# Kernel tuning notes

Hardware: AMD Instinct MI355X
Metric: run time of the kernel (lower is better)

Reference implementation:

```python
import jax, jax.numpy as jnp
import numpy as np
import math

D = 768      # inp_dim
NH = 8       # head_num
DH = 96      # head_dim
HID = NH * DH  # 768
P = 2 * D    # up_l proj dim = 1536
K = 4        # conv kernel size
CAP = 15.0   # gate soft cap
EPS = 1e-6


def layer_norm(x, w, b, eps=EPS):
    mu = jnp.mean(x, axis=-1, keepdims=True)
    var = jnp.mean((x - mu) ** 2, axis=-1, keepdims=True)
    return (x - mu) / jnp.sqrt(var + eps) * w + b


def softcap(v, cap=CAP):
    return cap * jnp.tanh(v / cap)


def setup_inputs() -> dict:
    key = jax.random.key(0)
    ks = jax.random.split(key, 8)
    B, S = 8, 2048
    x = jax.random.normal(ks[0], (B, S, D), dtype=jnp.float32)
    # scaled inits (1/sqrt(fan_in)) for numerical sanity
    up_l_w = jax.random.normal(ks[1], (P, D), dtype=jnp.float32) / math.sqrt(D)
    up_r_w = jax.random.normal(ks[2], (HID, D), dtype=jnp.float32) / math.sqrt(D)
    conv_w = jax.random.normal(ks[3], (K,), dtype=jnp.float32) / math.sqrt(K)
    skip_w = jax.random.normal(ks[4], (HID, P), dtype=jnp.float32) / math.sqrt(P)
    fused_w = jax.random.normal(ks[5], (2 * NH + 4 * HID, P), dtype=jnp.float32) / math.sqrt(P)
    fused_b = jnp.zeros((2 * NH + 4 * HID,), dtype=jnp.float32)
    down_w = jax.random.normal(ks[6], (D, HID), dtype=jnp.float32) / math.sqrt(HID)
    return {
        'x': x,
        'ln_w': jnp.ones((D,), jnp.float32), 'ln_b': jnp.zeros((D,), jnp.float32),
        'up_l_w': up_l_w, 'up_r_w': up_r_w, 'conv_w': conv_w, 'skip_w': skip_w,
        'fused_w': fused_w, 'fused_b': fused_b,
        'hid_w': jnp.ones((HID,), jnp.float32), 'hid_b': jnp.zeros((HID,), jnp.float32),
        'down_w': down_w,
    }


def reference(x, ln_w, ln_b, up_l_w, up_r_w, conv_w, skip_w, fused_w, fused_b, hid_w, hid_b, down_w):
    B, S, _ = x.shape
    dt = x.dtype
    inv_sqrt_dh = 1.0 / math.sqrt(DH)

    # ---- per-timestep-independent precomputation (vectorized over B,S) ----
    x_n = layer_norm(x, ln_w, ln_b)                       # [B,S,D]
    xl = jnp.einsum('bsd,pd->bsp', x_n, up_l_w)           # [B,S,P]
    r = jnp.einsum('bsd,hd->bsh', x_n, up_r_w)            # [B,S,HID]
    # causal conv over the FEATURE dim (Conv1d(1,1,K) applied to x_t.unsqueeze(1))
    xpad = jnp.pad(xl, ((0, 0), (0, 0), (K - 1, 0)))
    xc = conv_w[0] * xpad[..., 0:P]
    for t in range(1, K):
        xc = xc + conv_w[t] * xpad[..., t:t + P]
    xc = jax.nn.silu(xc)                                  # [B,S,P]
    x_skip = jnp.einsum('bsp,hp->bsh', xc, skip_w)        # [B,S,HID]
    z = jnp.einsum('bsp,op->bso', xc, fused_w) + fused_b  # [B,S,3088]
    i_g = softcap(z[..., :NH])                            # [B,S,NH]
    f_g = softcap(z[..., NH:2 * NH])                      # [B,S,NH]
    o = jax.nn.sigmoid(z[..., 2 * NH:2 * NH + HID])       # [B,S,HID]
    q = z[..., 2 * NH + HID:2 * NH + 2 * HID].reshape(B, S, NH, DH)
    k = z[..., 2 * NH + 2 * HID:2 * NH + 3 * HID].reshape(B, S, NH, DH) * inv_sqrt_dh
    v = z[..., 2 * NH + 3 * HID:].reshape(B, S, NH, DH)

    # ---- sequential matrix-state recurrence over time ----
    def step(carry, inp):
        c, n, m = carry
        it, ft, ot, qt, kt, vt, skipt, rt, xt = inp
        m_t = jnp.maximum(ft + m, it)                     # [B,NH]
        ig = jnp.exp(it - m_t)
        fg = jnp.exp(ft - m_t + m)
        c = fg[..., None, None] * c + ig[..., None, None] * jnp.einsum('bhd,bhe->bhde', vt, kt)
        n = fg[..., None] * n + ig[..., None] * kt
        num = jnp.einsum('bhde,bhe->bhd', c, qt)          # [B,NH,DH]
        den = jnp.maximum(jnp.sum(n * qt, axis=-1, keepdims=True), 1.0)
        h = ot * (num / den).reshape(B, HID)
        out = layer_norm(h, hid_w, hid_b) + skipt
        out = out * jax.nn.silu(rt)
        out = jnp.einsum('bh,dh->bd', out, down_w) + xt
        return (c, n, m_t), out

    tm = lambda a: jnp.swapaxes(a, 0, 1)  # time-major
    carry0 = (jnp.zeros((B, NH, DH, DH), dt), jnp.ones((B, NH, DH), dt), jnp.zeros((B, NH), dt))
    xs = (tm(i_g), tm(f_g), tm(o), tm(q), tm(k), tm(v), tm(x_skip), tm(r), tm(x))
    _, outs = jax.lax.scan(step, carry0, xs)
    return jnp.swapaxes(outs, 0, 1)  # [B,S,D]
```

## Files before the change

kernel.cpp:

```cpp
#include <hip/hip_runtime.h>
#include <hip/hip_bf16.h>

#define D_    768
#define P_    1536
#define HID_  768
#define NH_   8
#define DH_   96
#define S_    2048
#define LCH   256
#define NCH   8

typedef __hip_bfloat16 bf16_t;
typedef __attribute__((ext_vector_type(8))) short s16x8;
typedef __attribute__((ext_vector_type(8))) unsigned short u16x8;
typedef __attribute__((ext_vector_type(4))) float f32x4;

__device__ __forceinline__ float b2f(unsigned short u) {
    union { unsigned int i; float f; } x; x.i = ((unsigned int)u) << 16; return x.f;
}
__device__ __forceinline__ unsigned short f2b(float f) {
    bf16_t h = __float2bfloat16(f);
    unsigned short u; __builtin_memcpy(&u, &h, 2); return u;
}
__device__ __forceinline__ bf16_t u2b(unsigned short u) {
    bf16_t t; __builtin_memcpy(&t, &u, 2); return t;
}

__device__ __forceinline__ void gload16(const void* g, const void* l) {
    __builtin_amdgcn_global_load_lds(
        (const __attribute__((address_space(1))) unsigned int*)(unsigned long long)(g),
        (__attribute__((address_space(3))) unsigned int*)(unsigned int)(unsigned long long)(l),
        16, 0, 0);
}

__global__ void cvt_kernel(const float* __restrict__ src, bf16_t* __restrict__ dst, int n) {
    int i = blockIdx.x * blockDim.x + threadIdx.x;
    int stride = gridDim.x * blockDim.x;
    for (; i < n; i += stride) dst[i] = __float2bfloat16(src[i]);
}

__global__ void cvt2_kernel(const float* __restrict__ src, bf16_t* __restrict__ hi,
                            bf16_t* __restrict__ lo, int n) {
    int i = blockIdx.x * blockDim.x + threadIdx.x;
    int stride = gridDim.x * blockDim.x;
    for (; i < n; i += stride) {
        float x = src[i];
        bf16_t h = __float2bfloat16(x);
        hi[i] = h;
        lo[i] = __float2bfloat16(x - __bfloat162float(h));
    }
}

__global__ __launch_bounds__(256) void ln_x_kernel(const float* __restrict__ x,
                                                   const float* __restrict__ w,
                                                   const float* __restrict__ b,
                                                   bf16_t* __restrict__ xn) {
    const int t = blockIdx.x, tid = threadIdx.x;
    const size_t rb = (size_t)t * D_;
    float v0 = x[rb + tid], v1 = x[rb + tid + 256], v2 = x[rb + tid + 512];
    float sm = v0 + v1 + v2;
    float sq = v0 * v0 + v1 * v1 + v2 * v2;
#pragma unroll
    for (int off = 32; off > 0; off >>= 1) { sm += __shfl_xor(sm, off); sq += __shfl_xor(sq, off); }
    __shared__ float ws4[8];
    const int wid = tid >> 6, lane = tid & 63;
    if (lane == 0) { ws4[wid] = sm; ws4[4 + wid] = sq; }
    __syncthreads();
    sm = ws4[0] + ws4[1] + ws4[2] + ws4[3];
    sq = ws4[4] + ws4[5] + ws4[6] + ws4[7];
    const float mu = sm * (1.f / D_);
    const float rs = rsqrtf(sq * (1.f / D_) - mu * mu + 1e-6f);
    bf16_t* row = xn + (size_t)t * 1536;
#pragma unroll
    for (int k2 = 0; k2 < 3; ++k2) {
        const int c = tid + k2 * 256;
        const float v = (k2 == 0 ? v0 : k2 == 1 ? v1 : v2);
        const float y = (v - mu) * rs * w[c] + b[c];
        bf16_t h = __float2bfloat16(y);
        row[c] = h;
        row[768 + c] = __float2bfloat16(y - __bfloat162float(h));
    }
}

__global__ __launch_bounds__(192) void conv_gate_kernel(const float* __restrict__ xl,
                                                        const float* __restrict__ cw,
                                                        const float* __restrict__ fw,
                                                        const float* __restrict__ fb,
                                                        bf16_t* __restrict__ xch,
                                                        float* __restrict__ gates) {
    const int t = blockIdx.x, c = threadIdx.x;
    const float* row = xl + (size_t)t * P_;
    const float4* r4 = (const float4*)row;
    float4 a = r4[2 * c], b4 = r4[2 * c + 1];
    float pm3 = 0.f, pm2 = 0.f, pm1 = 0.f;
    if (c > 0) { pm3 = row[c * 8 - 3]; pm2 = row[c * 8 - 2]; pm1 = row[c * 8 - 1]; }
    const float w0 = cw[0], w1 = cw[1], w2 = cw[2], w3 = cw[3];
    float xv[11] = {pm3, pm2, pm1, a.x, a.y, a.z, a.w, b4.x, b4.y, b4.z, b4.w};
    float xc[8];
    u16x8 h8;
#pragma unroll
    for (int j = 0; j < 8; ++j) {
        float s = w0 * xv[j] + w1 * xv[j + 1] + w2 * xv[j + 2] + w3 * xv[j + 3];
        s = s * (1.f / (1.f + __expf(-s)));
        xc[j] = s;
        h8[j] = f2b(s);
    }
    *(u16x8*)(xch + (size_t)t * P_ + c * 8) = h8;

    float pj[16];
#pragma unroll
    for (int j = 0; j < 16; ++j) {
        const float* wr = fw + (size_t)j * P_ + c * 8;
        float p = 0.f;
#pragma unroll
        for (int u = 0; u < 8; ++u) p += xc[u] * wr[u];
        pj[j] = p;
    }
#pragma unroll
    for (int j = 0; j < 16; ++j)
#pragma unroll
        for (int off = 32; off > 0; off >>= 1) pj[j] += __shfl_xor(pj[j], off);
    __shared__ float red[3][16];
    const int wv = c >> 6, ln = c & 63;
    if (ln == 0) {
#pragma unroll
        for (int j = 0; j < 16; ++j) red[wv][j] = pj[j];
    }
    __syncthreads();
    if (c < 16) {
        const float z = red[0][c] + red[1][c] + red[2][c] + fb[c];
        gates[(size_t)t * 16 + c] = 15.f * tanhf(z * (1.f / 15.f));
    }
}

template <int NPASS, int MODE, int KTP>
__global__ __launch_bounds__(512, 2) void gemm256(
    const char* __restrict__ Ab, int astride, int aloff,
    const bf16_t* __restrict__ Wh, const bf16_t* __restrict__ Wl,
    bf16_t* __restrict__ out0, float* __restrict__ outf, int ldout,
    bf16_t* __restrict__ p1, bf16_t* __restrict__ p2,
    bf16_t* __restrict__ p3, bf16_t* __restrict__ p4,
    const float* __restrict__ bias, const float* __restrict__ resid) {
    __shared__ char smem[131072];
    const int tid = threadIdx.x;
    const int gx = gridDim.x;
    int flat = blockIdx.y * gx + blockIdx.x;
    const int cpx = (gx * gridDim.y) >> 3;
    flat = (flat & 7) * cpx + (flat >> 3);
    const int nt = flat % gx, mt = flat / gx;
    const int wid = tid >> 6, lane = tid & 63;
    const int wm = wid >> 2, wn = wid & 3;
    const int l15 = lane & 15, l4 = lane >> 4;
    const int sw = l15 & 7;
    constexpr int VT = NPASS * KTP;
    const size_t wstride = (size_t)KTP * 128;

    auto stage = [&](int h) {
        const int t = h >> 2;
        if (t >= VT) return;
        const int m = h & 3;
        const int pass = t / KTP;
        const int k0b = (t - pass * KTP) << 7;
        char* ldsdst = smem + (size_t)(h & 7) * 16384;
        const char* src;
        size_t stride;
        if (m < 2) {
            src = Ab + (pass == 2 ? aloff : 0) + (size_t)(mt * 256 + m * 128) * astride + k0b;
            stride = (size_t)astride;
        } else {
            const bf16_t* wp = (pass == 1) ? Wl : Wh;
            src = (const char*)wp + (size_t)(nt * 256 + (m - 2) * 128) * wstride + k0b;
            stride = wstride;
        }
        const int r0 = tid >> 3, cd = tid & 7;
#pragma unroll
        for (int l = 0; l < 2; ++l) {
            const int row = l * 64 + r0;
            gload16(src + (size_t)row * stride + (size_t)((cd ^ (row & 7)) << 4),
                    ldsdst + l * 8192 + tid * 16);
        }
    };

    f32x4 acc[8][4];
#pragma unroll
    for (int i = 0; i < 8; ++i)
#pragma unroll
        for (int j = 0; j < 4; ++j) acc[i][j] = f32x4{0.f, 0.f, 0.f, 0.f};

#pragma unroll
    for (int h = 0; h < 6; ++h) stage(h);
    asm volatile("s_waitcnt vmcnt(4)" ::: "memory");
    __builtin_amdgcn_s_barrier();

    s16x8 a03[4][2], a47[4][2], bb[2][2];

    for (int vt = 0; vt < VT; ++vt) {
        const char* ldsA = smem + (vt & 1) * 65536 + wm * 16384;
        const char* ldsB = smem + (vt & 1) * 65536 + 32768 + (wn >> 1) * 16384;
        const int brb = (wn & 1) * 64;
        const int hb = vt * 4 + 6;

#pragma unroll
        for (int i = 0; i < 4; ++i) {
            const int row = i * 16 + l15;
#pragma unroll
            for (int kk = 0; kk < 2; ++kk)
                a03[i][kk] = *(const s16x8*)(ldsA + row * 128 + ((((kk << 2) | l4) ^ sw) << 4));
        }
#pragma unroll
        for (int j = 0; j < 2; ++j) {
            const int row = brb + j * 16 + l15;
#pragma unroll
            for (int kk = 0; kk < 2; ++kk)
                bb[j][kk] = *(const s16x8*)(ldsB + row * 128 + ((((kk << 2) | l4) ^ sw) << 4));
        }
        stage(hb + 0);
        __builtin_amdgcn_s_barrier();
        __builtin_amdgcn_s_setprio(1);
#pragma unroll
        for (int i = 0; i < 4; ++i)
#pragma unroll
            for (int j = 0; j < 2; ++j)
#pragma unroll
                for (int kk = 0; kk < 2; ++kk)
                    acc[i][j] = __builtin_amdgcn_mfma_f32_16x16x32_bf16(a03[i][kk], bb[j][kk], acc[i][j], 0, 0, 0);
        __builtin_amdgcn_s_setprio(0);
        __builtin_amdgcn_s_barrier();

#pragma unroll
        for (int i = 0; i < 4; ++i) {
            const int row = (4 + i) * 16 + l15;
#pragma unroll
            for (int kk = 0; kk < 2; ++kk)
                a47[i][kk] = *(const s16x8*)(ldsA + row * 128 + ((((kk << 2) | l4) ^ sw) << 4));
        }
        stage(hb + 1);
        __builtin_amdgcn_s_barrier();
        __builtin_amdgcn_s_setprio(1);
#pragma unroll
        for (int i = 0; i < 4; ++i)
#pragma unroll
            for (int j = 0; j < 2; ++j)
#pragma unroll
                for (int kk = 0; kk < 2; ++kk)
                    acc[4 + i][j] = __builtin_amdgcn_mfma_f32_16x16x32_bf16(a47[i][kk], bb[j][kk], acc[4 + i][j], 0, 0, 0);
        __builtin_amdgcn_s_setprio(0);
        __builtin_amdgcn_s_barrier();

#pragma unroll
        for (int j = 0; j < 2; ++j) {
            const int row = brb + (2 + j) * 16 + l15;
#pragma unroll
            for (int kk = 0; kk < 2; ++kk)
                bb[j][kk] = *(const s16x8*)(ldsB + row * 128 + ((((kk << 2) | l4) ^ sw) << 4));
        }
        stage(hb + 2);
        __builtin_amdgcn_s_barrier();
        __builtin_amdgcn_s_setprio(1);
#pragma unroll
        for (int i = 0; i < 4; ++i)
#pragma unroll
            for (int j = 0; j < 2; ++j)
#pragma unroll
                for (int kk = 0; kk < 2; ++kk)
                    acc[4 + i][2 + j] = __builtin_amdgcn_mfma_f32_16x16x32_bf16(a47[i][kk], bb[j][kk], acc[4 + i][2 + j], 0, 0, 0);
        __builtin_amdgcn_s_setprio(0);
        __builtin_amdgcn_s_barrier();

        stage(hb + 3);
        __builtin_amdgcn_s_barrier();
        __builtin_amdgcn_s_setprio(1);
#pragma unroll
        for (int i = 0; i < 4; ++i)
#pragma unroll
            for (int j = 0; j < 2; ++j)
#pragma unroll
                for (int kk = 0; kk < 2; ++kk)
                    acc[i][2 + j] = __builtin_amdgcn_mfma_f32_16x16x32_bf16(a03[i][kk], bb[j][kk], acc[i][2 + j], 0, 0, 0);
        __builtin_amdgcn_s_setprio(0);
        asm volatile("s_waitcnt vmcnt(4)" ::: "memory");
        __builtin_amdgcn_s_barrier();
    }

    const int grow0 = mt * 256 + wm * 128;
    const int gcol0 = nt * 256 + wn * 64;
#pragma unroll
    for (int i = 0; i < 8; ++i) {
#pragma unroll
        for (int j = 0; j < 4; ++j) {
            const int gcol = gcol0 + j * 16 + l15;
#pragma unroll
            for (int r = 0; r < 4; ++r) {
                const int grow = grow0 + i * 16 + l4 * 4 + r;
                float v = acc[i][j][r];
                if constexpr (MODE == 0) {
                    out0[(size_t)grow * ldout + gcol] = __float2bfloat16(v);
                } else if constexpr (MODE == 1) {
                    outf[(size_t)grow * ldout + gcol] = v;
                } else if constexpr (MODE == 2) {
                    const int seg = gcol / 768;
                    const int col = gcol - seg * 768;
                    const size_t oo = (size_t)grow * 768 + col;
                    if (seg == 0) {
                        out0[oo] = __float2bfloat16(v);
                    } else {
                        v += bias[gcol - 768];
                        if (seg == 1)      p1[oo] = __float2bfloat16(1.f / (1.f + __expf(-v)));
                        else if (seg == 2) p2[oo] = __float2bfloat16(v);
                        else if (seg == 3) p3[oo] = __float2bfloat16(v * 0.10206207261596577f);
                        else               p4[oo] = __float2bfloat16(v);
                    }
                } else {
                    const size_t oo = (size_t)grow * ldout + gcol;
                    outf[oo] = v + resid[oo];
                }
            }
        }
    }
}

__global__ __launch_bounds__(64) void mscan_kernel(const float* __restrict__ gates,
                                                   float* __restrict__ wAo, float* __restrict__ go,
                                                   float* __restrict__ mprev, float* __restrict__ alpha) {
    const int b = blockIdx.x;
    const int lane = threadIdx.x;
    const int hd = lane >> 3, c = lane & 7;
    const size_t gbase = ((size_t)b * S_ + c * LCH) * 16;
    float F = 0.f, I = -1e30f;
    for (int t = 0; t < LCH; ++t) {
        const float fi = gates[gbase + t * 16 + hd];
        const float ff = gates[gbase + t * 16 + 8 + hd];
        I = fmaxf(I + ff, fi);
        F += ff;
    }
    float Fs = F, Is = I;
#pragma unroll
    for (int off = 1; off < 8; off <<= 1) {
        const float Fo = __shfl_up(Fs, off);
        const float Io = __shfl_up(Is, off);
        if (c >= off) { Is = fmaxf(Io + Fs, Is); Fs = Fo + Fs; }
    }
    const float Fe = __shfl_up(Fs, 1);
    const float Ie = __shfl_up(Is, 1);
    const float mp = (c == 0) ? 0.f : fmaxf(Fe, Ie);
    float m = mp; F = 0.f;
    const size_t wbase = ((size_t)(b * NH_ + hd)) * S_ + c * LCH;
    for (int t = 0; t < LCH; ++t) {
        const float fi = gates[gbase + t * 16 + hd];
        const float ff = gates[gbase + t * 16 + 8 + hd];
        F += ff;
        m = fmaxf(ff + m, fi);
        wAo[wbase + t] = fi - F;
        go[wbase + t] = F - m;
    }
    const int idx = (b * NH_ + hd) * NCH + c;
    mprev[idx] = mp;
    alpha[idx] = __expf(fminf(mp + F - m, 0.f));
}

__global__ __launch_bounds__(512) void chunkA_kernel(
    const bf16_t* __restrict__ kb, const bf16_t* __restrict__ vb,
    const float* __restrict__ wAo, const float* __restrict__ go,
    float* __restrict__ Bst) {
    const int c = blockIdx.x, bh = blockIdx.y;
    const int b = bh >> 3, hd = bh & 7;
    __shared__ bf16_t kT[96 * 136];
    __shared__ bf16_t vTh[96 * 136];
    __shared__ bf16_t vTl[96 * 136];
    __shared__ float coeffL[128];
    const int tid = threadIdx.x, lane = tid & 63, wid = tid >> 6;
    const int l15 = lane & 15, l4 = lane >> 4;
    const int s0 = c * LCH;
    const size_t seqb = (size_t)bh * S_;
    const float gend = go[seqb + s0 + LCH - 1];
    f32x4 acc[6];
#pragma unroll
    for (int nf = 0; nf < 6; ++nf) acc[nf] = f32x4{0.f, 0.f, 0.f, 0.f};
    float nacc = 0.f;
    const int ne = tid - 384;

    for (int sb = 0; sb < 2; ++sb) {
        __syncthreads();
        if (tid < 128) coeffL[tid] = __expf(fminf(wAo[seqb + s0 + sb * 128 + tid] + gend, 0.f));
        __syncthreads();
        {
            const int st = tid >> 2, e0 = (tid & 3) * 24;
            const size_t rowb = (size_t)(b * S_ + s0 + sb * 128 + st) * HID_ + hd * DH_ + e0;
            const float cf = coeffL[st];
#pragma unroll
            for (int jj = 0; jj < 3; ++jj) {
                const u16x8 kv = *(const u16x8*)(kb + rowb + jj * 8);
                const u16x8 vv = *(const u16x8*)(vb + rowb + jj * 8);
#pragma unroll
                for (int u = 0; u < 8; ++u) {
                    const int e = e0 + jj * 8 + u;
                    kT[e * 136 + st] = u2b(kv[u]);
                    const float vf = b2f(vv[u]) * cf;
                    const bf16_t hh = __float2bfloat16(vf);
                    vTh[e * 136 + st] = hh;
                    vTl[e * 136 + st] = __float2bfloat16(vf - __bfloat162float(hh));
                }
            }
        }
        __syncthreads();
        if (wid < 6) {
#pragma unroll
            for (int pass = 0; pass < 2; ++pass) {
                const bf16_t* Ap = pass ? vTl : vTh;
#pragma unroll
                for (int ks = 0; ks < 4; ++ks) {
                    const s16x8 af = *(const s16x8*)((const char*)Ap + (wid * 16 + l15) * 272 + ks * 64 + l4 * 16);
#pragma unroll
                    for (int nf = 0; nf < 6; ++nf) {
                        const s16x8 bf = *(const s16x8*)((const char*)kT + (nf * 16 + l15) * 272 + ks * 64 + l4 * 16);
                        acc[nf] = __builtin_amdgcn_mfma_f32_16x16x32_bf16(af, bf, acc[nf], 0, 0, 0);
                    }
                }
            }
        } else if (ne < 96) {
            for (int sg = 0; sg < 128; ++sg)
                nacc += coeffL[sg] * __bfloat162float(kT[ne * 136 + sg]);
        }
    }
    float* outp = Bst + ((size_t)bh * NCH + c) * 9312;
    if (wid < 6) {
#pragma unroll
        for (int nf = 0; nf < 6; ++nf)
#pragma unroll
            for (int r = 0; r < 4; ++r)
                outp[(size_t)(wid * 16 + l4 * 4 + r) * 96 + nf * 16 + l15] = acc[nf][r];
    } else if (ne < 96) {
        outp[9216 + ne] = nacc;
    }
}

__global__ __launch_bounds__(96) void chunkB_kernel(float* __restrict__ Bst,
                                                    const float* __restrict__ alpha) {
    const int idx = blockIdx.x * 96 + threadIdx.x;
    const int bh = blockIdx.y;
    float val = (idx < 9216) ? 0.f : 1.f;
    for (int c = 0; c < NCH; ++c) {
        float* p = Bst + ((size_t)bh * NCH + c) * 9312 + idx;
        const float t = *p;
        *p = val;
        val = alpha[bh * NCH + c] * val + t;
    }
}

__global__ __launch_bounds__(256) void chunkC_kernel(
    const bf16_t* __restrict__ qb, const bf16_t* __restrict__ kb,
    const bf16_t* __restrict__ vb, const bf16_t* __restrict__ ob,
    const float* __restrict__ wAo, const float* __restrict__ go,
    const float* __restrict__ mprev, const float* __restrict__ Cst,
    float* __restrict__ hb) {
    const int c = blockIdx.x >> 2, qblk = blockIdx.x & 3;
    const int bh = blockIdx.y, b = bh >> 3, hd = bh & 7;
    __shared__ bf16_t Qs[64 * 104];
    __shared__ bf16_t Ks[64 * 104];
    __shared__ bf16_t vTs[112 * 72];
    __shared__ bf16_t Phs[64 * 72];
    __shared__ bf16_t Pls[64 * 72];
    __shared__ bf16_t CsH[112 * 104];
    __shared__ bf16_t CsL[112 * 104];
    __shared__ float wAL[256];
    __shared__ float gL[64];
    __shared__ float scL[64];
    const int tid = threadIdx.x, lane = tid & 63, wid = tid >> 6;
    const int l15 = lane & 15, l4 = lane >> 4;
    const int s0 = c * LCH;
    const size_t seqb = (size_t)bh * S_;
    const int tq0 = b * S_ + s0 + qblk * 64;

    wAL[tid] = wAo[seqb + s0 + tid];
    if (tid < 64) {
        const float gg = go[seqb + s0 + qblk * 64 + tid];
        gL[tid] = gg;
        scL[tid] = __expf(fminf(mprev[bh * NCH + c] + gg, 0.f));
    }
    {
        const int tt = tid >> 2, e0 = (tid & 3) * 24;
        const bf16_t* qrow = qb + (size_t)(tq0 + tt) * HID_ + hd * DH_ + e0;
#pragma unroll
        for (int jj = 0; jj < 3; ++jj)
            *(u16x8*)&Qs[tt * 104 + e0 + jj * 8] = *(const u16x8*)(qrow + jj * 8);
    }
    {
        const float* Csp = Cst + ((size_t)bh * NCH + c) * 9312;
        for (int i = tid; i < 9312; i += 256) {
            int dd, ee;
            if (i < 9216) { dd = i / 96; ee = i - dd * 96; }
            else          { dd = 96;     ee = i - 9216; }
            const float xv = Csp[i];
            const bf16_t hh = __float2bfloat16(xv);
            CsH[dd * 104 + ee] = hh;
            CsL[dd * 104 + ee] = __float2bfloat16(xv - __bfloat162float(hh));
        }
        const bf16_t z16 = __float2bfloat16(0.f);
        for (int i = tid; i < 15 * 104; i += 256) { CsH[97 * 104 + i] = z16; CsL[97 * 104 + i] = z16; }
        if (tid < 64) vTs[96 * 72 + tid] = __float2bfloat16(1.f);
        for (int i = tid; i < 15 * 72; i += 256) vTs[97 * 72 + i] = z16;
    }
    __syncthreads();

    f32x4 acc[7];
#pragma unroll
    for (int nf = 0; nf < 7; ++nf) acc[nf] = f32x4{0.f, 0.f, 0.f, 0.f};
#pragma unroll
    for (int pass = 0; pass < 2; ++pass) {
        const bf16_t* Cp = pass ? CsL : CsH;
#pragma unroll
        for (int ks = 0; ks < 3; ++ks) {
            const s16x8 af = *(const s16x8*)((const char*)Qs + (wid * 16 + l15) * 208 + ks * 64 + l4 * 16);
#pragma unroll
            for (int nf = 0; nf < 7; ++nf) {
                const s16x8 bf = *(const s16x8*)((const char*)Cp + (nf * 16 + l15) * 208 + ks * 64 + l4 * 16);
                acc[nf] = __builtin_amdgcn_mfma_f32_16x16x32_bf16(af, bf, acc[nf], 0, 0, 0);
            }
        }
    }
    {
        float scr[4];
#pragma unroll
        for (int r = 0; r < 4; ++r) scr[r] = scL[wid * 16 + l4 * 4 + r];
#pragma unroll
        for (int nf = 0; nf < 7; ++nf)
#pragma unroll
            for (int r = 0; r < 4; ++r) acc[nf][r] *= scr[r];
    }

    for (int sb = 0; sb <= qblk; ++sb) {
        __syncthreads();
        {
            const int tt = tid >> 2, e0 = (tid & 3) * 24;
            const size_t rowb = (size_t)(b * S_ + s0 + sb * 64 + tt) * HID_ + hd * DH_ + e0;
#pragma unroll
            for (int jj = 0; jj < 3; ++jj) {
                *(u16x8*)&Ks[tt * 104 + e0 + jj * 8] = *(const u16x8*)(kb + rowb + jj * 8);
                const u16x8 vv = *(const u16x8*)(vb + rowb + jj * 8);
#pragma unroll
                for (int u = 0; u < 8; ++u)
                    vTs[(e0 + jj * 8 + u) * 72 + tt] = u2b(vv[u]);
            }
        }
        __syncthreads();
        f32x4 pacc[4];
#pragma unroll
        for (int nf = 0; nf < 4; ++nf) pacc[nf] = f32x4{0.f, 0.f, 0.f, 0.f};
#pragma unroll
        for (int ks = 0; ks < 3; ++ks) {
            const s16x8 af = *(const s16x8*)((const char*)Qs + (wid * 16 + l15) * 208 + ks * 64 + l4 * 16);
#pragma unroll
            for (int nf = 0; nf < 4; ++nf) {
                const s16x8 bf = *(const s16x8*)((const char*)Ks + (nf * 16 + l15) * 208 + ks * 64 + l4 * 16);
                pacc[nf] = __builtin_amdgcn_mfma_f32_16x16x32_bf16(af, bf, pacc[nf], 0, 0, 0);
            }
        }
#pragma unroll
        for (int nf = 0; nf < 4; ++nf) {
#pragma unroll
            for (int r = 0; r < 4; ++r) {
                const int tr = wid * 16 + l4 * 4 + r;
                const int sg = nf * 16 + l15;
                float p = 0.f;
                if (sb < qblk || sg <= tr)
                    p = pacc[nf][r] * __expf(fminf(wAL[sb * 64 + sg] + gL[tr], 0.f));
                const bf16_t hh = __float2bfloat16(p);
                Phs[tr * 72 + sg] = hh;
                Pls[tr * 72 + sg] = __float2bfloat16(p - __bfloat162float(hh));
            }
        }
        __syncthreads();
#pragma unroll
        for (int pass = 0; pass < 2; ++pass) {
            const bf16_t* Pp = pass ? Pls : Phs;
#pragma unroll
            for (int ks = 0; ks < 2; ++ks) {
                const s16x8 af = *(const s16x8*)((const char*)Pp + (wid * 16 + l15) * 144 + ks * 64 + l4 * 16);
#pragma unroll
                for (int nf = 0; nf < 7; ++nf) {
                    const s16x8 bf = *(const s16x8*)((const char*)vTs + (nf * 16 + l15) * 144 + ks * 64 + l4 * 16);
                    acc[nf] = __builtin_amdgcn_mfma_f32_16x16x32_bf16(af, bf, acc[nf], 0, 0, 0);
                }
            }
        }
    }

#pragma unroll
    for (int r = 0; r < 4; ++r) {
        float den = __shfl(acc[6][r], lane & 48);
        den = fmaxf(den, 1.0f);
        const int tr = wid * 16 + l4 * 4 + r;
        const size_t rowb = (size_t)(tq0 + tr) * HID_ + hd * DH_;
#pragma unroll
        for (int nf = 0; nf < 6; ++nf) {
            const int dc = nf * 16 + l15;
            const float o = __bfloat162float(ob[rowb + dc]);
            hb[rowb + dc] = o * acc[nf][r] / den;
        }
    }
}

__global__ __launch_bounds__(256) void epi1_kernel(const float* __restrict__ h,
                                                   const bf16_t* __restrict__ xskip,
                                                   const bf16_t* __restrict__ r,
                                                   const float* __restrict__ hw,
                                                   const float* __restrict__ hbi,
                                                   bf16_t* __restrict__ pre) {
    const int t = blockIdx.x, tid = threadIdx.x;
    const size_t rb = (size_t)t * HID_;
    float v0 = h[rb + tid], v1 = h[rb + tid + 256], v2 = h[rb + tid + 512];
    float sm = v0 + v1 + v2;
    float sq = v0 * v0 + v1 * v1 + v2 * v2;
#pragma unroll
    for (int off = 32; off > 0; off >>= 1) { sm += __shfl_xor(sm, off); sq += __shfl_xor(sq, off); }
    __shared__ float ws4[8];
    const int wid = tid >> 6, lane = tid & 63;
    if (lane == 0) { ws4[wid] = sm; ws4[4 + wid] = sq; }
    __syncthreads();
    sm = ws4[0] + ws4[1] + ws4[2] + ws4[3];
    sq = ws4[4] + ws4[5] + ws4[6] + ws4[7];
    const float mu = sm * (1.f / HID_);
    const float rs = rsqrtf(sq * (1.f / HID_) - mu * mu + 1e-6f);
    bf16_t* row = pre + (size_t)t * HID_;
#pragma unroll
    for (int k2 = 0; k2 < 3; ++k2) {
        const int c = tid + k2 * 256;
        const float v = (k2 == 0 ? v0 : k2 == 1 ? v1 : v2);
        float o = (v - mu) * rs * hw[c] + hbi[c] + __bfloat162float(xskip[rb + c]);
        const float rv = __bfloat162float(r[rb + c]);
        o *= rv * (1.f / (1.f + __expf(-rv)));
        row[c] = __float2bfloat16(o);
    }
}

extern "C" void kernel_launch(void* const* d_in, const int* in_sizes, int n_in,
                              void* d_out, int out_size, void* d_ws, size_t ws_size,
                              hipStream_t stream) {
    const float* x      = (const float*)d_in[0];
    const float* ln_w   = (const float*)d_in[1];
    const float* ln_b   = (const float*)d_in[2];
    const float* up_l_w = (const float*)d_in[3];
    const float* up_r_w = (const float*)d_in[4];
    const float* conv_w = (const float*)d_in[5];
    const float* skip_w = (const float*)d_in[6];
    const float* fused_w= (const float*)d_in[7];
    const float* fused_b= (const float*)d_in[8];
    const float* hid_w  = (const float*)d_in[9];
    const float* hid_b  = (const float*)d_in[10];
    const float* down_w = (const float*)d_in[11];
    float* out = (float*)d_out;
    (void)n_in; (void)out_size; (void)ws_size;

    const size_t T = (size_t)in_sizes[0] / D_;
    const int B = (int)(T / S_);

    char* ws = (char*)d_ws;
    size_t off = 0;
    auto take = [&](size_t bytes) -> char* {
        char* p = ws + off; off = (off + bytes + 255) & ~(size_t)255; return p;
    };
    char* arena = take(20123904);
    bf16_t* wul_h = (bf16_t*)(arena);
    bf16_t* wul_l = (bf16_t*)(arena + 2359296);
    bf16_t* wur   = (bf16_t*)(arena + 4718592);
    bf16_t* wcat  = (bf16_t*)(arena + 5898240);
    float* Bst    = (float*)(arena);
    float* wAarr  = (float*)(arena + 19071232);
    float* garr   = (float*)(arena + 19595520);
    float* mprevA = (float*)(arena + 20119808);
    float* alphaA = (float*)(arena + 20121856);

    bf16_t* wdn_h = (bf16_t*)take((size_t)D_ * HID_ * 2);
    char*   xnreg = take(T * 1536 * 2);
    char*   big   = take(T * 1536 * 4);
    bf16_t* rbuf  = (bf16_t*)take(T * HID_ * 2);
    bf16_t* skipb = (bf16_t*)take(T * HID_ * 2);
    float*  gates = (float*)take(T * 16 * 4);

    bf16_t* xn   = (bf16_t*)xnreg;
    bf16_t* xch  = (bf16_t*)xnreg;
    float*  h    = (float*)xnreg;
    float*  xl   = (float*)big;
    bf16_t* obuf = (bf16_t*)big;
    bf16_t* qbuf = (bf16_t*)(big + T * HID_ * 2);
    bf16_t* kbuf = (bf16_t*)(big + T * HID_ * 4);
    bf16_t* vbuf = (bf16_t*)(big + T * HID_ * 6);
    bf16_t* pre  = (bf16_t*)big;

    const int MT = (int)(T / 256);

    cvt2_kernel<<<512, 256, 0, stream>>>(up_l_w, wul_h, wul_l, P_ * D_);
    cvt_kernel <<<512, 256, 0, stream>>>(up_r_w, wur, HID_ * D_);
    cvt_kernel <<<512, 256, 0, stream>>>(skip_w, wcat, HID_ * P_);
    cvt_kernel <<<2048, 256, 0, stream>>>(fused_w + (size_t)16 * P_, wcat + (size_t)HID_ * P_, 3072 * P_);
    cvt_kernel <<<512, 256, 0, stream>>>(down_w, wdn_h, D_ * HID_);
    ln_x_kernel<<<(int)T, 256, 0, stream>>>(x, ln_w, ln_b, xn);
    gemm256<3, 1, 12><<<dim3(P_ / 256, MT), 512, 0, stream>>>(
        (const char*)xn, 3072, 1536, wul_h, wul_l,
        nullptr, xl, P_, nullptr, nullptr, nullptr, nullptr, nullptr, nullptr);
    gemm256<1, 0, 12><<<dim3(HID_ / 256, MT), 512, 0, stream>>>(
        (const char*)xn, 3072, 0, wur, nullptr,
        rbuf, nullptr, HID_, nullptr, nullptr, nullptr, nullptr, nullptr, nullptr);
    conv_gate_kernel<<<(int)T, 192, 0, stream>>>(xl, conv_w, fused_w, fused_b, xch, gates);
    gemm256<1, 2, 24><<<dim3(3840 / 256, MT), 512, 0, stream>>>(
        (const char*)xch, 3072, 0, wcat, nullptr,
        skipb, nullptr, 0, obuf, qbuf, kbuf, vbuf, fused_b + 16, nullptr);
    mscan_kernel<<<B, 64, 0, stream>>>(gates, wAarr, garr, mprevA, alphaA);
    chunkA_kernel<<<dim3(NCH, B * NH_), 512, 0, stream>>>(kbuf, vbuf, wAarr, garr, Bst);
    chunkB_kernel<<<dim3(97, B * NH_), 96, 0, stream>>>(Bst, alphaA);
    chunkC_kernel<<<dim3(NCH * 4, B * NH_), 256, 0, stream>>>(qbuf, kbuf, vbuf, obuf,
                                                              wAarr, garr, mprevA, Bst, h);
    epi1_kernel<<<(int)T, 256, 0, stream>>>(h, skipb, rbuf, hid_w, hid_b, pre);
    gemm256<1, 3, 12><<<dim3(HID_ / 256, MT), 512, 0, stream>>>(
        (const char*)pre, 1536, 0, wdn_h, nullptr,
        nullptr, out, HID_, nullptr, nullptr, nullptr, nullptr, nullptr, x);
}
```

Before: 822.6 us.

## Drop split-bf16 compensation passes and merge up-projection GEMMs and weight casts

Removes the hi/lo bf16 split used to emulate higher precision in the layer-norm output, chunk-state accumulation and intra-chunk attention, so each of those MFMA loops runs a single pass. The two up-projection GEMMs are merged into one launch with a new output mode that writes float xl and bf16 r. The weight-cast kernels are folded into one launch, and the normalizer vector in chunkA is computed by MFMA through an extra coefficient row instead of a scalar loop. This cuts MFMA work, LDS use and launches, at the cost of lower numerical precision in the recurrence.

```diff
diff --git a/kernel.cpp b/kernel.cpp
--- a/kernel.cpp
+++ b/kernel.cpp
@@ -33,21 +33,27 @@
         16, 0, 0);
 }
 
-__global__ void cvt_kernel(const float* __restrict__ src, bf16_t* __restrict__ dst, int n) {
+__global__ void cvt_all_kernel(const float* __restrict__ up_l_w, const float* __restrict__ up_r_w,
+                               const float* __restrict__ skip_w, const float* __restrict__ fused_w,
+                               const float* __restrict__ down_w,
+                               bf16_t* __restrict__ win_h, bf16_t* __restrict__ win_l,
+                               bf16_t* __restrict__ wcat, bf16_t* __restrict__ wdn) {
+    const int N1 = 2304 * 768, N2 = 3840 * 1536, N3 = 768 * 768;
     int i = blockIdx.x * blockDim.x + threadIdx.x;
-    int stride = gridDim.x * blockDim.x;
-    for (; i < n; i += stride) dst[i] = __float2bfloat16(src[i]);
-}
-
-__global__ void cvt2_kernel(const float* __restrict__ src, bf16_t* __restrict__ hi,
-                            bf16_t* __restrict__ lo, int n) {
-    int i = blockIdx.x * blockDim.x + threadIdx.x;
-    int stride = gridDim.x * blockDim.x;
-    for (; i < n; i += stride) {
-        float x = src[i];
-        bf16_t h = __float2bfloat16(x);
-        hi[i] = h;
-        lo[i] = __float2bfloat16(x - __bfloat162float(h));
+    const int stride = gridDim.x * blockDim.x;
+    for (; i < N1 + N2 + N3; i += stride) {
+        if (i < N1) {
+            const float x = (i < 1536 * 768) ? up_l_w[i] : up_r_w[i - 1536 * 768];
+            const bf16_t h = __float2bfloat16(x);
+            win_h[i] = h;
+            win_l[i] = __float2bfloat16(x - __bfloat162float(h));
+        } else if (i < N1 + N2) {
+            const int j = i - N1;
+            const float x = (j < 768 * 1536) ? skip_w[j] : fused_w[16 * 1536 + (j - 768 * 1536)];
+            wcat[j] = __float2bfloat16(x);
+        } else {
+            wdn[i - N1 - N2] = __float2bfloat16(down_w[i - N1 - N2]);
+        }
     }
 }
 
@@ -70,15 +76,12 @@
     sq = ws4[4] + ws4[5] + ws4[6] + ws4[7];
     const float mu = sm * (1.f / D_);
     const float rs = rsqrtf(sq * (1.f / D_) - mu * mu + 1e-6f);
-    bf16_t* row = xn + (size_t)t * 1536;
+    bf16_t* row = xn + rb;
 #pragma unroll
     for (int k2 = 0; k2 < 3; ++k2) {
         const int c = tid + k2 * 256;
         const float v = (k2 == 0 ? v0 : k2 == 1 ? v1 : v2);
-        const float y = (v - mu) * rs * w[c] + b[c];
-        bf16_t h = __float2bfloat16(y);
-        row[c] = h;
-        row[768 + c] = __float2bfloat16(y - __bfloat162float(h));
+        row[c] = __float2bfloat16((v - mu) * rs * w[c] + b[c]);
     }
 }
 
@@ -310,9 +313,12 @@
                         else if (seg == 3) p3[oo] = __float2bfloat16(v * 0.10206207261596577f);
                         else               p4[oo] = __float2bfloat16(v);
                     }
-                } else {
+                } else if constexpr (MODE == 3) {
                     const size_t oo = (size_t)grow * ldout + gcol;
                     outf[oo] = v + resid[oo];
+                } else {
+                    if (gcol < 1536) outf[(size_t)grow * 1536 + gcol] = v;
+                    else             out0[(size_t)grow * 768 + (gcol - 1536)] = __float2bfloat16(v);
                 }
             }
         }
@@ -365,8 +371,7 @@
     const int c = blockIdx.x, bh = blockIdx.y;
     const int b = bh >> 3, hd = bh & 7;
     __shared__ bf16_t kT[96 * 136];
-    __shared__ bf16_t vTh[96 * 136];
-    __shared__ bf16_t vTl[96 * 136];
+    __shared__ bf16_t vTh[112 * 136];
     __shared__ float coeffL[128];
     const int tid = threadIdx.x, lane = tid & 63, wid = tid >> 6;
     const int l15 = lane & 15, l4 = lane >> 4;
@@ -376,12 +381,19 @@
     f32x4 acc[6];
 #pragma unroll
     for (int nf = 0; nf < 6; ++nf) acc[nf] = f32x4{0.f, 0.f, 0.f, 0.f};
-    float nacc = 0.f;
-    const int ne = tid - 384;
+
+    {
+        const bf16_t z16 = __float2bfloat16(0.f);
+        for (int i = tid; i < 15 * 136; i += 512) vTh[97 * 136 + i] = z16;
+    }
 
     for (int sb = 0; sb < 2; ++sb) {
         __syncthreads();
-        if (tid < 128) coeffL[tid] = __expf(fminf(wAo[seqb + s0 + sb * 128 + tid] + gend, 0.f));
+        if (tid < 128) {
+            const float cf = __expf(fminf(wAo[seqb + s0 + sb * 128 + tid] + gend, 0.f));
+            coeffL[tid] = cf;
+            vTh[96 * 136 + tid] = __float2bfloat16(cf);
+        }
         __syncthreads();
         {
             const int st = tid >> 2, e0 = (tid & 3) * 24;
@@ -395,31 +407,21 @@
                 for (int u = 0; u < 8; ++u) {
                     const int e = e0 + jj * 8 + u;
                     kT[e * 136 + st] = u2b(kv[u]);
-                    const float vf = b2f(vv[u]) * cf;
-                    const bf16_t hh = __float2bfloat16(vf);
-                    vTh[e * 136 + st] = hh;
-                    vTl[e * 136 + st] = __float2bfloat16(vf - __bfloat162float(hh));
+                    vTh[e * 136 + st] = __float2bfloat16(b2f(vv[u]) * cf);
                 }
             }
         }
         __syncthreads();
-        if (wid < 6) {
-#pragma unroll
-            for (int pass = 0; pass < 2; ++pass) {
-                const bf16_t* Ap = pass ? vTl : vTh;
-#pragma unroll
-                for (int ks = 0; ks < 4; ++ks) {
-                    const s16x8 af = *(const s16x8*)((const char*)Ap + (wid * 16 + l15) * 272 + ks * 64 + l4 * 16);
-#pragma unroll
-                    for (int nf = 0; nf < 6; ++nf) {
-                        const s16x8 bf = *(const s16x8*)((const char*)kT + (nf * 16 + l15) * 272 + ks * 64 + l4 * 16);
-                        acc[nf] = __builtin_amdgcn_mfma_f32_16x16x32_bf16(af, bf, acc[nf], 0, 0, 0);
-                    }
+        if (wid < 7) {
+#pragma unroll
+            for (int ks = 0; ks < 4; ++ks) {
+                const s16x8 af = *(const s16x8*)((const char*)vTh + (wid * 16 + l15) * 272 + ks * 64 + l4 * 16);
+#pragma unroll
+                for (int nf = 0; nf < 6; ++nf) {
+                    const s16x8 bf = *(const s16x8*)((const char*)kT + (nf * 16 + l15) * 272 + ks * 64 + l4 * 16);
+                    acc[nf] = __builtin_amdgcn_mfma_f32_16x16x32_bf16(af, bf, acc[nf], 0, 0, 0);
                 }
             }
-        } else if (ne < 96) {
-            for (int sg = 0; sg < 128; ++sg)
-                nacc += coeffL[sg] * __bfloat162float(kT[ne * 136 + sg]);
         }
     }
     float* outp = Bst + ((size_t)bh * NCH + c) * 9312;
@@ -429,8 +431,10 @@
 #pragma unroll
             for (int r = 0; r < 4; ++r)
                 outp[(size_t)(wid * 16 + l4 * 4 + r) * 96 + nf * 16 + l15] = acc[nf][r];
-    } else if (ne < 96) {
-        outp[9216 + ne] = nacc;
+    } else if (wid == 6 && l4 == 0) {
+#pragma unroll
+        for (int nf = 0; nf < 6; ++nf)
+            outp[9216 + nf * 16 + l15] = acc[nf][0];
     }
 }
 
@@ -459,9 +463,7 @@
     __shared__ bf16_t Ks[64 * 104];
     __shared__ bf16_t vTs[112 * 72];
     __shared__ bf16_t Phs[64 * 72];
-    __shared__ bf16_t Pls[64 * 72];
     __shared__ bf16_t CsH[112 * 104];
-    __shared__ bf16_t CsL[112 * 104];
     __shared__ float wAL[256];
     __shared__ float gL[64];
     __shared__ float scL[64];
@@ -490,13 +492,10 @@
             int dd, ee;
             if (i < 9216) { dd = i / 96; ee = i - dd * 96; }
             else          { dd = 96;     ee = i - 9216; }
-            const float xv = Csp[i];
-            const bf16_t hh = __float2bfloat16(xv);
-            CsH[dd * 104 + ee] = hh;
-            CsL[dd * 104 + ee] = __float2bfloat16(xv - __bfloat162float(hh));
+            CsH[dd * 104 + ee] = __float2bfloat16(Csp[i]);
         }
         const bf16_t z16 = __float2bfloat16(0.f);
-        for (int i = tid; i < 15 * 104; i += 256) { CsH[97 * 104 + i] = z16; CsL[97 * 104 + i] = z16; }
+        for (int i = tid; i < 15 * 104; i += 256) CsH[97 * 104 + i] = z16;
         if (tid < 64) vTs[96 * 72 + tid] = __float2bfloat16(1.f);
         for (int i = tid; i < 15 * 72; i += 256) vTs[97 * 72 + i] = z16;
     }
@@ -506,16 +505,12 @@
 #pragma unroll
     for (int nf = 0; nf < 7; ++nf) acc[nf] = f32x4{0.f, 0.f, 0.f, 0.f};
 #pragma unroll
-    for (int pass = 0; pass < 2; ++pass) {
-        const bf16_t* Cp = pass ? CsL : CsH;
-#pragma unroll
-        for (int ks = 0; ks < 3; ++ks) {
-            const s16x8 af = *(const s16x8*)((const char*)Qs + (wid * 16 + l15) * 208 + ks * 64 + l4 * 16);
-#pragma unroll
-            for (int nf = 0; nf < 7; ++nf) {
-                const s16x8 bf = *(const s16x8*)((const char*)Cp + (nf * 16 + l15) * 208 + ks * 64 + l4 * 16);
-                acc[nf] = __builtin_amdgcn_mfma_f32_16x16x32_bf16(af, bf, acc[nf], 0, 0, 0);
-            }
+    for (int ks = 0; ks < 3; ++ks) {
+        const s16x8 af = *(const s16x8*)((const char*)Qs + (wid * 16 + l15) * 208 + ks * 64 + l4 * 16);
+#pragma unroll
+        for (int nf = 0; nf < 7; ++nf) {
+            const s16x8 bf = *(const s16x8*)((const char*)CsH + (nf * 16 + l15) * 208 + ks * 64 + l4 * 16);
+            acc[nf] = __builtin_amdgcn_mfma_f32_16x16x32_bf16(af, bf, acc[nf], 0, 0, 0);
         }
     }
     {
@@ -564,23 +559,17 @@
                 float p = 0.f;
                 if (sb < qblk || sg <= tr)
                     p = pacc[nf][r] * __expf(fminf(wAL[sb * 64 + sg] + gL[tr], 0.f));
-                const bf16_t hh = __float2bfloat16(p);
-                Phs[tr * 72 + sg] = hh;
-                Pls[tr * 72 + sg] = __float2bfloat16(p - __bfloat162float(hh));
+                Phs[tr * 72 + sg] = __float2bfloat16(p);
             }
         }
         __syncthreads();
 #pragma unroll
-        for (int pass = 0; pass < 2; ++pass) {
-            const bf16_t* Pp = pass ? Pls : Phs;
-#pragma unroll
-            for (int ks = 0; ks < 2; ++ks) {
-                const s16x8 af = *(const s16x8*)((const char*)Pp + (wid * 16 + l15) * 144 + ks * 64 + l4 * 16);
-#pragma unroll
-                for (int nf = 0; nf < 7; ++nf) {
-                    const s16x8 bf = *(const s16x8*)((const char*)vTs + (nf * 16 + l15) * 144 + ks * 64 + l4 * 16);
-                    acc[nf] = __builtin_amdgcn_mfma_f32_16x16x32_bf16(af, bf, acc[nf], 0, 0, 0);
-                }
+        for (int ks = 0; ks < 2; ++ks) {
+            const s16x8 af = *(const s16x8*)((const char*)Phs + (wid * 16 + l15) * 144 + ks * 64 + l4 * 16);
+#pragma unroll
+            for (int nf = 0; nf < 7; ++nf) {
+                const s16x8 bf = *(const s16x8*)((const char*)vTs + (nf * 16 + l15) * 144 + ks * 64 + l4 * 16);
+                acc[nf] = __builtin_amdgcn_mfma_f32_16x16x32_bf16(af, bf, acc[nf], 0, 0, 0);
             }
         }
     }
@@ -660,10 +649,9 @@
         char* p = ws + off; off = (off + bytes + 255) & ~(size_t)255; return p;
     };
     char* arena = take(20123904);
-    bf16_t* wul_h = (bf16_t*)(arena);
-    bf16_t* wul_l = (bf16_t*)(arena + 2359296);
-    bf16_t* wur   = (bf16_t*)(arena + 4718592);
-    bf16_t* wcat  = (bf16_t*)(arena + 5898240);
+    bf16_t* win_h = (bf16_t*)(arena);
+    bf16_t* win_l = (bf16_t*)(arena + 3538944);
+    bf16_t* wcat  = (bf16_t*)(arena + 7077888);
     float* Bst    = (float*)(arena);
     float* wAarr  = (float*)(arena + 19071232);
     float* garr   = (float*)(arena + 19595520);
@@ -689,18 +677,12 @@
 
     const int MT = (int)(T / 256);
 
-    cvt2_kernel<<<512, 256, 0, stream>>>(up_l_w, wul_h, wul_l, P_ * D_);
-    cvt_kernel <<<512, 256, 0, stream>>>(up_r_w, wur, HID_ * D_);
-    cvt_kernel <<<512, 256, 0, stream>>>(skip_w, wcat, HID_ * P_);
-    cvt_kernel <<<2048, 256, 0, stream>>>(fused_w + (size_t)16 * P_, wcat + (size_t)HID_ * P_, 3072 * P_);
-    cvt_kernel <<<512, 256, 0, stream>>>(down_w, wdn_h, D_ * HID_);
+    cvt_all_kernel<<<2048, 256, 0, stream>>>(up_l_w, up_r_w, skip_w, fused_w, down_w,
+                                             win_h, win_l, wcat, wdn_h);
     ln_x_kernel<<<(int)T, 256, 0, stream>>>(x, ln_w, ln_b, xn);
-    gemm256<3, 1, 12><<<dim3(P_ / 256, MT), 512, 0, stream>>>(
-        (const char*)xn, 3072, 1536, wul_h, wul_l,
-        nullptr, xl, P_, nullptr, nullptr, nullptr, nullptr, nullptr, nullptr);
-    gemm256<1, 0, 12><<<dim3(HID_ / 256, MT), 512, 0, stream>>>(
-        (const char*)xn, 3072, 0, wur, nullptr,
-        rbuf, nullptr, HID_, nullptr, nullptr, nullptr, nullptr, nullptr, nullptr);
+    gemm256<2, 4, 12><<<dim3(2304 / 256, MT), 512, 0, stream>>>(
+        (const char*)xn, 1536, 0, win_h, win_l,
+        rbuf, xl, 0, nullptr, nullptr, nullptr, nullptr, nullptr, nullptr);
     conv_gate_kernel<<<(int)T, 192, 0, stream>>>(xl, conv_w, fused_w, fused_b, xch, gates);
     gemm256<1, 2, 24><<<dim3(3840 / 256, MT), 512, 0, stream>>>(
         (const char*)xch, 3072, 0, wcat, nullptr,
```

Result: faster. 721.4 us (-12.3%).
